# Optimization experiments

Hardware: AMD Instinct MI355X
Metric: run time of the kernel (lower is better)

Reference implementation:

```python
import jax, jax.numpy as jnp
import numpy as np

TS = 1.5          # hard-coded sampling period in forward()
W_CENTER = 337.927  # hard-coded center frequency in forward()


def shg_mat(yta):
    """Vectorized createSHGmat: yta is a complex64 vector of length N.
    Row m: Ts * fftshift(fft(fftshift(yta * roll(yta, delay[m]) * shiftFactor))).
    torch.roll(x, s)[j] == x[(j - s) % N], matching the gather below."""
    N = yta.shape[0]
    delays_f = jnp.arange(-(N // 2), N // 2, dtype=jnp.float32)
    delays_i = jnp.arange(-(N // 2), N // 2, dtype=jnp.int32)
    shift_factor = jnp.exp(-1j * 2.0 * W_CENTER * TS * delays_f).astype(jnp.complex64)  # [N]
    idx = (jnp.arange(N, dtype=jnp.int32)[None, :] - delays_i[:, None]) % N  # [N, N]
    y_shift = yta[idx]                                    # [N(delay), N(elem)]
    prod = yta[None, :] * y_shift * shift_factor[None, :]  # elementwise, [N, N]
    prod = jnp.fft.fftshift(prod, axes=-1)
    mat = TS * jnp.fft.fftshift(jnp.fft.fft(prod, axis=-1), axes=-1)
    return mat  # complex64 [N, N]


def frog_error(Tref, Tmeas):
    """calcFrogError: scalar FROG error between reference and measured traces."""
    mu = jnp.sum(Tmeas @ Tref) / jnp.sum(Tref @ Tref)
    r = jnp.sum((Tmeas - mu * Tref) ** 2)
    norm = jnp.float32(Tmeas.size) * jnp.max(Tmeas) ** 2
    return jnp.sqrt(r / norm)


def setup_inputs() -> dict:
    key = jax.random.key(0)
    k1, k2, k3 = jax.random.split(key, 3)
    B, N = 8, 1024
    prediction = jax.random.normal(k1, (B, 2 * N), dtype=jnp.float32)
    label = jax.random.normal(k2, (B, 2 * N), dtype=jnp.float32)
    spectrogram = jax.random.uniform(k3, (N, N), dtype=jnp.float32)
    return {"prediction": prediction, "label": label, "spectrogram": spectrogram}


def reference(prediction, label, spectrogram):
    B, two_n = prediction.shape
    n = two_n // 2
    pred_analytical = (prediction[:, :n] + 1j * prediction[:, n:]).astype(jnp.complex64)  # [B, N]
    mats = jax.vmap(shg_mat)(pred_analytical)          # [B, N, N] complex64
    Tref = jnp.abs(mats)                               # predicted SHG trace magnitude
    errs = jax.vmap(lambda t: frog_error(t, spectrogram))(Tref)  # [B]
    # loss = (sum over batch of frog_error) / batch_size; masked MSE terms in the
    # original are computed but never added to the returned loss, so they are omitted.
    return jnp.mean(errs)
```

## Files before the change

### kernel.cpp

```cpp
#include <hip/hip_runtime.h>
#include <math.h>

#define N 1024
#define B_ 8
#define T_ 512
#define NREP 4
#define CHUNKS 64

#define OFF_SF      0
#define OFF_TA      2048
#define OFF_TB      4096
#define OFF_ROWSUM  4224
#define ZERO_START  12416
#define OFF_COLSUMM 12416
#define OFF_SUMM2   13440
#define OFF_MAXM    13441
#define OFF_SUMMT   13448
#define OFF_SUMTT   13456
#define OFF_COLT    13464
#define WS_END      (OFF_COLT + B_ * NREP * N)

__device__ __forceinline__ float wave_sum(float v) {
    #pragma unroll
    for (int o = 32; o > 0; o >>= 1) v += __shfl_down(v, o, 64);
    return v;
}
__device__ __forceinline__ float wave_max(float v) {
    #pragma unroll
    for (int o = 32; o > 0; o >>= 1) v = fmaxf(v, __shfl_down(v, o, 64));
    return v;
}

__device__ __forceinline__ void cmul(float& xr, float& xi, float wr, float wi) {
    float r = xr * wr - xi * wi;
    float i = xr * wi + xi * wr;
    xr = r; xi = i;
}

__device__ __forceinline__ void dft4(float& r0, float& i0, float& r1, float& i1,
                                     float& r2, float& i2, float& r3, float& i3) {
    float e0r = r0 + r2, e0i = i0 + i2;
    float e1r = r0 - r2, e1i = i0 - i2;
    float e2r = r1 + r3, e2i = i1 + i3;
    float e3r = r1 - r3, e3i = i1 - i3;
    r0 = e0r + e2r; i0 = e0i + e2i;
    r2 = e0r - e2r; i2 = e0i - e2i;
    r1 = e1r + e3i; i1 = e1i - e3r;
    r3 = e1r - e3i; i3 = e1i + e3r;
}

__device__ __forceinline__ void dft16(float xr[16], float xi[16]) {
    #pragma unroll
    for (int b = 0; b < 4; ++b)
        dft4(xr[b], xi[b], xr[4 + b], xi[4 + b], xr[8 + b], xi[8 + b], xr[12 + b], xi[12 + b]);
    const float C1 = 0.9238795325112867f, S1 = 0.3826834323650898f;
    const float C2 = 0.7071067811865476f;
    cmul(xr[5],  xi[5],   C1, -S1);
    cmul(xr[6],  xi[6],   C2, -C2);
    cmul(xr[7],  xi[7],   S1, -C1);
    cmul(xr[9],  xi[9],   C2, -C2);
    { float t = xr[10]; xr[10] = xi[10]; xi[10] = -t; }
    cmul(xr[11], xi[11], -C2, -C2);
    cmul(xr[13], xi[13],  S1, -C1);
    cmul(xr[14], xi[14], -C2, -C2);
    cmul(xr[15], xi[15], -C1,  S1);
    #pragma unroll
    for (int c = 0; c < 4; ++c)
        dft4(xr[4 * c], xi[4 * c], xr[4 * c + 1], xi[4 * c + 1],
             xr[4 * c + 2], xi[4 * c + 2], xr[4 * c + 3], xi[4 * c + 3]);
}

template<int CTRL>
__device__ __forceinline__ float dppf(float x) {
    return __int_as_float(__builtin_amdgcn_update_dpp(
        0, __float_as_int(x), CTRL, 0xF, 0xF, true));
}
#define DPP_XOR1 0xB1
#define DPP_XOR2 0x4E

__global__ __launch_bounds__(256) void k_prep(float* ws) {
    const int e = blockIdx.x * 256 + threadIdx.x;
    if (e < 1024) {
        double ang = -2.0 * 337.927 * 1.5 * (double)(e - 512);
        double s, c;
        sincos(ang, &s, &c);
        ws[OFF_SF + 2 * e]     = (float)c;
        ws[OFF_SF + 2 * e + 1] = (float)s;
    } else if (e < 2048) {
        int e2 = e - 1024;
        int k1 = e2 >> 6, uu = e2 & 63;
        double ang = -2.0 * M_PI * (double)(uu * k1) / 1024.0;
        double s, c;
        sincos(ang, &s, &c);
        ws[OFF_TA + 2 * e2]     = (float)c;
        ws[OFF_TA + 2 * e2 + 1] = (float)s;
    } else if (e < 2112) {
        int e2 = e - 2048;
        int k2 = e2 >> 2, n3 = e2 & 3;
        double ang = -2.0 * M_PI * (double)(n3 * k2) / 64.0;
        double s, c;
        sincos(ang, &s, &c);
        ws[OFF_TB + 2 * e2]     = (float)c;
        ws[OFF_TB + 2 * e2 + 1] = (float)s;
    }
}

__global__ __attribute__((amdgpu_flat_work_group_size(T_, T_), amdgpu_waves_per_eu(2, 4)))
void k_row(const float* __restrict__ pred,
           const float* __restrict__ M,
           float* __restrict__ ws) {
    __shared__ float2 Y2[N];
    __shared__ float2 TPh[8][N / 2];
    __shared__ float2 sfL[N];
    __shared__ float2 taL[N];
    __shared__ float2 TB2[64];
    __shared__ float  colAcc[N];
    __shared__ float  redf[2][8];
    const int t = threadIdx.x;
    const int cnk = blockIdx.x;
    const int y = blockIdx.y;
    const int wid = t >> 6, u = t & 63;

    if (y == 0) {
        const int r0 = cnk * 16;
        float cs0 = 0.f, cs1 = 0.f, sq = 0.f, mx = 0.f;
        for (int r = 0; r < 16; ++r) {
            const float* row = M + (size_t)(r0 + r) * N;
            float v0 = row[t], v1 = row[t + 512];
            cs0 += v0; cs1 += v1;
            sq += v0 * v0 + v1 * v1;
            mx = fmaxf(mx, fmaxf(v0, v1));
        }
        atomicAdd(&ws[OFF_COLSUMM + t],       cs0);
        atomicAdd(&ws[OFF_COLSUMM + t + 512], cs1);
        sq = wave_sum(sq);
        mx = wave_max(mx);
        if (u == 0) { redf[0][wid] = sq; redf[1][wid] = mx; }
        __syncthreads();
        if (t == 0) {
            float ssq = 0.f, smx = 0.f;
            #pragma unroll
            for (int i = 0; i < 8; ++i) { ssq += redf[0][i]; smx = fmaxf(smx, redf[1][i]); }
            atomicAdd(&ws[OFF_SUMM2], ssq);
            atomicMax((unsigned int*)ws + OFF_MAXM, __float_as_uint(smx));
        }
        return;
    }
    const int b = y - 1;

    {
        const float* pr = pred + (size_t)b * 2 * N;
        float2 re = *(const float2*)(pr + 2 * t);
        float2 im = *(const float2*)(pr + N + 2 * t);
        Y2[2 * t]     = make_float2(re.x, im.x);
        Y2[2 * t + 1] = make_float2(re.y, im.y);
        const float2* g = (const float2*)ws;
        sfL[t]       = g[OFF_SF / 2 + t];
        sfL[t + 512] = g[OFF_SF / 2 + t + 512];
        taL[t]       = g[OFF_TA / 2 + t];
        taL[t + 512] = g[OFF_TA / 2 + t + 512];
        if (t < 64) TB2[t] = g[OFF_TB / 2 + t];
        colAcc[t] = 0.f;
        colAcc[t + 512] = 0.f;
    }
    __syncthreads();

    const int k1u = u >> 2;
    const int n3 = u & 3;
    const int k3 = ((u & 1) << 1) | ((u >> 1) & 1);
    const int clane = (k1u | (k3 << 8)) ^ 512;
    const bool hi2 = (u & 2) != 0;
    const bool odd = (u & 1) != 0;
    float2* tp = TPh[wid];

    float mtl = 0.f, ttl = 0.f;
    const int nrow = (cnk == 0 && wid == 0) ? 2 : 1;

    for (int rr = 0; rr < nrow; ++rr) {
        const int m = (rr == 0) ? (cnk * 8 + wid) : 512;
        const int mm = (N - m) & (N - 1);
        const bool domm = (mm != m);
        const float w = domm ? 2.f : 1.f;
        const float mmw = domm ? 1.f : 0.f;

        float xr[16], xi[16];
        const int sbase = (u - m + 512) & (N - 1);
        #pragma unroll
        for (int n1 = 0; n1 < 16; ++n1) {
            int j = (n1 << 6) + u;
            float2 yj = Y2[j];
            float2 sv = sfL[j];
            int s = (sbase + (n1 << 6)) & (N - 1);
            float2 yb = Y2[s];
            float ar = yj.x * sv.x - yj.y * sv.y;
            float ai = yj.x * sv.y + yj.y * sv.x;
            xr[n1] = ar * yb.x - ai * yb.y;
            xi[n1] = ar * yb.y + ai * yb.x;
        }
        dft16(xr, xi);
        #pragma unroll
        for (int r = 1; r < 16; ++r) {
            int k1 = ((r & 3) << 2) | (r >> 2);
            float2 wv = taL[(k1 << 6) + u];
            cmul(xr[r], xi[r], wv.x, wv.y);
        }

        float yr[16], yi[16];
        asm volatile("s_waitcnt lgkmcnt(0)" ::: "memory");
        #pragma unroll
        for (int r = 0; r < 16; ++r) if ((r & 3) < 2) {
            int k1 = ((r & 3) << 2) | (r >> 2);
            int el = ((k1 & 7) << 6) | (((k1u ^ k1) & 15) << 2) | n3;
            tp[el] = make_float2(xr[r], xi[r]);
        }
        asm volatile("s_waitcnt lgkmcnt(0)" ::: "memory");
        if (u < 32) {
            #pragma unroll
            for (int n2 = 0; n2 < 16; ++n2) {
                int el = ((k1u & 7) << 6) | (((n2 ^ k1u) & 15) << 2) | n3;
                float2 v = tp[el];
                yr[n2] = v.x; yi[n2] = v.y;
            }
        }
        asm volatile("s_waitcnt lgkmcnt(0)" ::: "memory");
        #pragma unroll
        for (int r = 0; r < 16; ++r) if ((r & 3) >= 2) {
            int k1 = ((r & 3) << 2) | (r >> 2);
            int el = ((k1 & 7) << 6) | (((k1u ^ k1) & 15) << 2) | n3;
            tp[el] = make_float2(xr[r], xi[r]);
        }
        asm volatile("s_waitcnt lgkmcnt(0)" ::: "memory");
        if (u >= 32) {
            #pragma unroll
            for (int n2 = 0; n2 < 16; ++n2) {
                int el = ((k1u & 7) << 6) | (((n2 ^ k1u) & 15) << 2) | n3;
                float2 v = tp[el];
                yr[n2] = v.x; yi[n2] = v.y;
            }
        }

        dft16(yr, yi);
        #pragma unroll
        for (int r = 1; r < 16; ++r) {
            int k2 = ((r & 3) << 2) | (r >> 2);
            float2 wv = TB2[(k2 << 2) | n3];
            cmul(yr[r], yi[r], wv.x, wv.y);
        }

        const float* Mrow  = M + (size_t)m * N + clane;
        const float* Mrow2 = M + (size_t)mm * N + clane;
        const float w225 = w * 2.25f;
        float rs = 0.f;
        #pragma unroll
        for (int r = 0; r < 16; ++r) {
            int k2 = ((r & 3) << 2) | (r >> 2);
            float ar = yr[r], ai = yi[r];
            float br = dppf<DPP_XOR2>(ar), bi = dppf<DPP_XOR2>(ai);
            float zr = hi2 ? (br - ar) : (ar + br);
            float zi = hi2 ? (bi - ai) : (ai + bi);
            float qr = dppf<DPP_XOR1>(zr), qi = dppf<DPP_XOR1>(zi);
            float Xr = odd ? (qr - (hi2 ? zi : zr)) : (zr + (hi2 ? qi : qr));
            float Xi = odd ? (qi + (hi2 ? zr : -zi)) : (zi + (hi2 ? -qr : qi));
            float mag2 = Xr * Xr + Xi * Xi;
            float v = 1.5f * sqrtf(mag2);
            rs  += v;
            ttl += w225 * mag2;
            float ms = Mrow[k2 << 4] + mmw * Mrow2[k2 << 4];
            mtl += ms * v;
            int cc = clane + (k2 << 4);
            atomicAdd(&colAcc[cc ^ ((cc >> 4) & 16)], w * v);
        }
        rs = wave_sum(rs);
        if (u == 0) {
            ws[OFF_ROWSUM + (size_t)b * N + m] = rs;
            if (domm) ws[OFF_ROWSUM + (size_t)b * N + mm] = rs;
        }
    }

    mtl = wave_sum(mtl);
    ttl = wave_sum(ttl);
    if (u == 0) { redf[0][wid] = mtl; redf[1][wid] = ttl; }
    __syncthreads();
    if (t == 0) {
        float smt = 0.f, stt = 0.f;
        #pragma unroll
        for (int i = 0; i < 8; ++i) { smt += redf[0][i]; stt += redf[1][i]; }
        atomicAdd(&ws[OFF_SUMMT + b], smt);
        atomicAdd(&ws[OFF_SUMTT + b], stt);
    }
    {
        float* colT = ws + OFF_COLT + (size_t)(b * NREP + (cnk & (NREP - 1))) * N;
        int j = t;
        atomicAdd(&colT[j], colAcc[j ^ ((j >> 4) & 16)]);
        j = t + 512;
        atomicAdd(&colT[j], colAcc[j ^ ((j >> 4) & 16)]);
    }
}

__global__ __launch_bounds__(256) void k_final(float* ws, float* out) {
    __shared__ double redn[4], redd[4];
    const int b = blockIdx.x;
    const int t = threadIdx.x;
    const int wid = t >> 6, lane = t & 63;
    const float* rowsum = ws + OFF_ROWSUM + (size_t)b * N;
    double num = 0.0, den = 0.0;
    #pragma unroll
    for (int q = 0; q < 4; ++q) {
        int j = t + 256 * q;
        double r = (double)rowsum[j];
        float ct = 0.f;
        #pragma unroll
        for (int rep = 0; rep < NREP; ++rep)
            ct += ws[OFF_COLT + (size_t)(b * NREP + rep) * N + j];
        num += (double)ws[OFF_COLSUMM + j] * r;
        den += (double)ct * r;
    }
    #pragma unroll
    for (int o = 32; o > 0; o >>= 1) {
        num += __shfl_down(num, o, 64);
        den += __shfl_down(den, o, 64);
    }
    if (lane == 0) { redn[wid] = num; redd[wid] = den; }
    __syncthreads();
    if (t == 0) {
        double NUM = redn[0] + redn[1] + redn[2] + redn[3];
        double DEN = redd[0] + redd[1] + redd[2] + redd[3];
        double mu = NUM / DEN;
        double r = (double)ws[OFF_SUMM2] - 2.0 * mu * (double)ws[OFF_SUMMT + b]
                 + mu * mu * (double)ws[OFF_SUMTT + b];
        float mx = ws[OFF_MAXM];
        double norm = 1048576.0 * (double)mx * (double)mx;
        atomicAdd(out, (float)(sqrt(r / norm) / 8.0));
    }
}

extern "C" void kernel_launch(void* const* d_in, const int* in_sizes, int n_in,
                              void* d_out, int out_size, void* d_ws, size_t ws_size,
                              hipStream_t stream) {
    const float* pred = (const float*)d_in[0];
    const float* M = (const float*)d_in[2];
    float* ws = (float*)d_ws;
    float* out = (float*)d_out;

    hipMemsetAsync(ws + ZERO_START, 0, (size_t)(WS_END - ZERO_START) * sizeof(float), stream);
    hipMemsetAsync(out, 0, sizeof(float), stream);
    k_prep<<<9, 256, 0, stream>>>(ws);
    dim3 grid(CHUNKS, B_ + 1);
    k_row<<<grid, T_, 0, stream>>>(pred, M, ws);
    k_final<<<B_, 256, 0, stream>>>(ws, out);
}
```

Before: 106.0 us.

## Precompute y*shift-factor in LDS, vectorize complex math, prefetch spectrogram rows early

Folds the shift-factor multiply into a per-block precomputed Ysf array, so each row's product needs one complex multiply instead of two. Rewrites the FFT butterflies and complex multiplies with 2-wide float vectors so the compiler can emit packed FP32 ops. Moves the global loads of the spectrogram rows ahead of the LDS transpose, overlapping their latency with the FFT work and skipping the mirror-row load when it is not needed. The prefetched values cost 32 extra registers, which may reduce occupancy.

```diff
diff --git a/kernel.cpp b/kernel.cpp
--- a/kernel.cpp
+++ b/kernel.cpp
@@ -20,6 +20,41 @@
 #define OFF_COLT    13464
 #define WS_END      (OFF_COLT + B_ * NREP * N)
 
+typedef float f2 __attribute__((ext_vector_type(2)));
+__device__ __forceinline__ f2 mkf2(float a, float b) { f2 r; r.x = a; r.y = b; return r; }
+
+__device__ __forceinline__ f2 cmulv(f2 a, f2 b) {
+    f2 p = mkf2(a.x, a.x) * b;
+    f2 q = mkf2(a.y, a.y) * mkf2(b.y, b.x);
+    return mkf2(p.x - q.x, p.y + q.y);
+}
+
+__device__ __forceinline__ void dft4v(f2& a0, f2& a1, f2& a2, f2& a3) {
+    f2 e0 = a0 + a2, e1 = a0 - a2, e2 = a1 + a3, e3 = a1 - a3;
+    a0 = e0 + e2;
+    a2 = e0 - e2;
+    a1 = mkf2(e1.x + e3.y, e1.y - e3.x);
+    a3 = mkf2(e1.x - e3.y, e1.y + e3.x);
+}
+
+__device__ __forceinline__ void dft16v(f2 x[16]) {
+    #pragma unroll
+    for (int b = 0; b < 4; ++b) dft4v(x[b], x[4 + b], x[8 + b], x[12 + b]);
+    const float C1 = 0.9238795325112867f, S1 = 0.3826834323650898f;
+    const float C2 = 0.7071067811865476f;
+    x[5]  = cmulv(x[5],  mkf2( C1, -S1));
+    x[6]  = cmulv(x[6],  mkf2( C2, -C2));
+    x[7]  = cmulv(x[7],  mkf2( S1, -C1));
+    x[9]  = cmulv(x[9],  mkf2( C2, -C2));
+    x[10] = mkf2(x[10].y, -x[10].x);
+    x[11] = cmulv(x[11], mkf2(-C2, -C2));
+    x[13] = cmulv(x[13], mkf2( S1, -C1));
+    x[14] = cmulv(x[14], mkf2(-C2, -C2));
+    x[15] = cmulv(x[15], mkf2(-C1,  S1));
+    #pragma unroll
+    for (int c = 0; c < 4; ++c) dft4v(x[4*c], x[4*c+1], x[4*c+2], x[4*c+3]);
+}
+
 __device__ __forceinline__ float wave_sum(float v) {
     #pragma unroll
     for (int o = 32; o > 0; o >>= 1) v += __shfl_down(v, o, 64);
@@ -29,45 +64,6 @@
     #pragma unroll
     for (int o = 32; o > 0; o >>= 1) v = fmaxf(v, __shfl_down(v, o, 64));
     return v;
-}
-
-__device__ __forceinline__ void cmul(float& xr, float& xi, float wr, float wi) {
-    float r = xr * wr - xi * wi;
-    float i = xr * wi + xi * wr;
-    xr = r; xi = i;
-}
-
-__device__ __forceinline__ void dft4(float& r0, float& i0, float& r1, float& i1,
-                                     float& r2, float& i2, float& r3, float& i3) {
-    float e0r = r0 + r2, e0i = i0 + i2;
-    float e1r = r0 - r2, e1i = i0 - i2;
-    float e2r = r1 + r3, e2i = i1 + i3;
-    float e3r = r1 - r3, e3i = i1 - i3;
-    r0 = e0r + e2r; i0 = e0i + e2i;
-    r2 = e0r - e2r; i2 = e0i - e2i;
-    r1 = e1r + e3i; i1 = e1i - e3r;
-    r3 = e1r - e3i; i3 = e1i + e3r;
-}
-
-__device__ __forceinline__ void dft16(float xr[16], float xi[16]) {
-    #pragma unroll
-    for (int b = 0; b < 4; ++b)
-        dft4(xr[b], xi[b], xr[4 + b], xi[4 + b], xr[8 + b], xi[8 + b], xr[12 + b], xi[12 + b]);
-    const float C1 = 0.9238795325112867f, S1 = 0.3826834323650898f;
-    const float C2 = 0.7071067811865476f;
-    cmul(xr[5],  xi[5],   C1, -S1);
-    cmul(xr[6],  xi[6],   C2, -C2);
-    cmul(xr[7],  xi[7],   S1, -C1);
-    cmul(xr[9],  xi[9],   C2, -C2);
-    { float t = xr[10]; xr[10] = xi[10]; xi[10] = -t; }
-    cmul(xr[11], xi[11], -C2, -C2);
-    cmul(xr[13], xi[13],  S1, -C1);
-    cmul(xr[14], xi[14], -C2, -C2);
-    cmul(xr[15], xi[15], -C1,  S1);
-    #pragma unroll
-    for (int c = 0; c < 4; ++c)
-        dft4(xr[4 * c], xi[4 * c], xr[4 * c + 1], xi[4 * c + 1],
-             xr[4 * c + 2], xi[4 * c + 2], xr[4 * c + 3], xi[4 * c + 3]);
 }
 
 template<int CTRL>
@@ -109,13 +105,13 @@
 void k_row(const float* __restrict__ pred,
            const float* __restrict__ M,
            float* __restrict__ ws) {
-    __shared__ float2 Y2[N];
-    __shared__ float2 TPh[8][N / 2];
-    __shared__ float2 sfL[N];
-    __shared__ float2 taL[N];
-    __shared__ float2 TB2[64];
-    __shared__ float  colAcc[N];
-    __shared__ float  redf[2][8];
+    __shared__ f2   Y2[N];
+    __shared__ f2   Ysf[N];
+    __shared__ f2   taL[N];
+    __shared__ f2   TPh[8][N / 2];
+    __shared__ f2   TB2[64];
+    __shared__ float colAcc[N];
+    __shared__ float redf[2][8];
     const int t = threadIdx.x;
     const int cnk = blockIdx.x;
     const int y = blockIdx.y;
@@ -152,11 +148,12 @@
         const float* pr = pred + (size_t)b * 2 * N;
         float2 re = *(const float2*)(pr + 2 * t);
         float2 im = *(const float2*)(pr + N + 2 * t);
-        Y2[2 * t]     = make_float2(re.x, im.x);
-        Y2[2 * t + 1] = make_float2(re.y, im.y);
-        const float2* g = (const float2*)ws;
-        sfL[t]       = g[OFF_SF / 2 + t];
-        sfL[t + 512] = g[OFF_SF / 2 + t + 512];
+        const f2* g = (const f2*)ws;
+        f2 y0 = mkf2(re.x, im.x), y1 = mkf2(re.y, im.y);
+        Y2[2 * t]     = y0;
+        Y2[2 * t + 1] = y1;
+        Ysf[2 * t]     = cmulv(y0, g[OFF_SF / 2 + 2 * t]);
+        Ysf[2 * t + 1] = cmulv(y1, g[OFF_SF / 2 + 2 * t + 1]);
         taL[t]       = g[OFF_TA / 2 + t];
         taL[t + 512] = g[OFF_TA / 2 + t + 512];
         if (t < 64) TB2[t] = g[OFF_TB / 2 + t];
@@ -171,7 +168,7 @@
     const int clane = (k1u | (k3 << 8)) ^ 512;
     const bool hi2 = (u & 2) != 0;
     const bool odd = (u & 1) != 0;
-    float2* tp = TPh[wid];
+    f2* tp = TPh[wid];
 
     float mtl = 0.f, ttl = 0.f;
     const int nrow = (cnk == 0 && wid == 0) ? 2 : 1;
@@ -183,43 +180,54 @@
         const float w = domm ? 2.f : 1.f;
         const float mmw = domm ? 1.f : 0.f;
 
-        float xr[16], xi[16];
+        f2 x[16];
         const int sbase = (u - m + 512) & (N - 1);
         #pragma unroll
         for (int n1 = 0; n1 < 16; ++n1) {
             int j = (n1 << 6) + u;
-            float2 yj = Y2[j];
-            float2 sv = sfL[j];
             int s = (sbase + (n1 << 6)) & (N - 1);
-            float2 yb = Y2[s];
-            float ar = yj.x * sv.x - yj.y * sv.y;
-            float ai = yj.x * sv.y + yj.y * sv.x;
-            xr[n1] = ar * yb.x - ai * yb.y;
-            xi[n1] = ar * yb.y + ai * yb.x;
-        }
-        dft16(xr, xi);
+            x[n1] = cmulv(Ysf[j], Y2[s]);
+        }
+        dft16v(x);
         #pragma unroll
         for (int r = 1; r < 16; ++r) {
             int k1 = ((r & 3) << 2) | (r >> 2);
-            float2 wv = taL[(k1 << 6) + u];
-            cmul(xr[r], xi[r], wv.x, wv.y);
-        }
-
-        float yr[16], yi[16];
+            x[r] = cmulv(x[r], taL[(k1 << 6) + u]);
+        }
+
+        const float* Mrow  = M + (size_t)m * N + clane;
+        const float* Mrow2 = M + (size_t)mm * N + clane;
+        float mrA[16], mrB[16];
+        #pragma unroll
+        for (int r = 0; r < 16; ++r) {
+            int k2 = ((r & 3) << 2) | (r >> 2);
+            mrA[r] = Mrow[k2 << 4];
+        }
+        if (domm) {
+            #pragma unroll
+            for (int r = 0; r < 16; ++r) {
+                int k2 = ((r & 3) << 2) | (r >> 2);
+                mrB[r] = Mrow2[k2 << 4];
+            }
+        } else {
+            #pragma unroll
+            for (int r = 0; r < 16; ++r) mrB[r] = 0.f;
+        }
+
+        f2 yv[16];
         asm volatile("s_waitcnt lgkmcnt(0)" ::: "memory");
         #pragma unroll
         for (int r = 0; r < 16; ++r) if ((r & 3) < 2) {
             int k1 = ((r & 3) << 2) | (r >> 2);
             int el = ((k1 & 7) << 6) | (((k1u ^ k1) & 15) << 2) | n3;
-            tp[el] = make_float2(xr[r], xi[r]);
+            tp[el] = x[r];
         }
         asm volatile("s_waitcnt lgkmcnt(0)" ::: "memory");
         if (u < 32) {
             #pragma unroll
             for (int n2 = 0; n2 < 16; ++n2) {
                 int el = ((k1u & 7) << 6) | (((n2 ^ k1u) & 15) << 2) | n3;
-                float2 v = tp[el];
-                yr[n2] = v.x; yi[n2] = v.y;
+                yv[n2] = tp[el];
             }
         }
         asm volatile("s_waitcnt lgkmcnt(0)" ::: "memory");
@@ -227,34 +235,30 @@
         for (int r = 0; r < 16; ++r) if ((r & 3) >= 2) {
             int k1 = ((r & 3) << 2) | (r >> 2);
             int el = ((k1 & 7) << 6) | (((k1u ^ k1) & 15) << 2) | n3;
-            tp[el] = make_float2(xr[r], xi[r]);
+            tp[el] = x[r];
         }
         asm volatile("s_waitcnt lgkmcnt(0)" ::: "memory");
         if (u >= 32) {
             #pragma unroll
             for (int n2 = 0; n2 < 16; ++n2) {
                 int el = ((k1u & 7) << 6) | (((n2 ^ k1u) & 15) << 2) | n3;
-                float2 v = tp[el];
-                yr[n2] = v.x; yi[n2] = v.y;
+                yv[n2] = tp[el];
             }
         }
 
-        dft16(yr, yi);
+        dft16v(yv);
         #pragma unroll
         for (int r = 1; r < 16; ++r) {
             int k2 = ((r & 3) << 2) | (r >> 2);
-            float2 wv = TB2[(k2 << 2) | n3];
-            cmul(yr[r], yi[r], wv.x, wv.y);
-        }
-
-        const float* Mrow  = M + (size_t)m * N + clane;
-        const float* Mrow2 = M + (size_t)mm * N + clane;
+            yv[r] = cmulv(yv[r], TB2[(k2 << 2) | n3]);
+        }
+
         const float w225 = w * 2.25f;
         float rs = 0.f;
         #pragma unroll
         for (int r = 0; r < 16; ++r) {
             int k2 = ((r & 3) << 2) | (r >> 2);
-            float ar = yr[r], ai = yi[r];
+            float ar = yv[r].x, ai = yv[r].y;
             float br = dppf<DPP_XOR2>(ar), bi = dppf<DPP_XOR2>(ai);
             float zr = hi2 ? (br - ar) : (ar + br);
             float zi = hi2 ? (bi - ai) : (ai + bi);
@@ -265,7 +269,7 @@
             float v = 1.5f * sqrtf(mag2);
             rs  += v;
             ttl += w225 * mag2;
-            float ms = Mrow[k2 << 4] + mmw * Mrow2[k2 << 4];
+            float ms = mrA[r] + mmw * mrB[r];
             mtl += ms * v;
             int cc = clane + (k2 << 4);
             atomicAdd(&colAcc[cc ^ ((cc >> 4) & 16)], w * v);
```

Measured after the change: 107.2 us. No clear change (+1.1%).
